# Kernel tuning notes

Measured on AMD Instinct MI355X. Metric: run time of the kernel, lower is better.

Reference implementation:

```python
import jax, jax.numpy as jnp
import numpy as np

B, T, D, H, F = 2, 128, 256, 8, 64
C = H * F          # channels = 512
TEMB = 512         # time_embed_dim


def setup_inputs() -> dict:
    key = jax.random.key(0)
    ks = jax.random.split(key, 9)
    qk = jax.random.normal(ks[0], (B, D, H, T, F), jnp.float32)
    # integer-valued relative distances in [-(T-1), T-1], stored as float
    pairwise_distances = jax.random.randint(ks[1], (B, T, T), -(T - 1), T).astype(jnp.float32)
    temb = jax.random.normal(ks[2], (B, T, TEMB), jnp.float32)
    # linear layer params (note: original zero-inits w_out/b_out; we use random
    # values so the kernel correctness test is non-trivial)
    w_dist = jax.random.normal(ks[3], (C, 3), jnp.float32) / np.sqrt(3.0)
    b_dist = jax.random.normal(ks[4], (C,), jnp.float32) * 0.02
    w_time = jax.random.normal(ks[5], (C, TEMB), jnp.float32) / np.sqrt(TEMB)
    b_time = jax.random.normal(ks[6], (C,), jnp.float32) * 0.02
    w_out = jax.random.normal(ks[7], (C, C), jnp.float32) / np.sqrt(C)
    b_out = jax.random.normal(ks[8], (C,), jnp.float32) * 0.02
    return {"qk": qk, "pairwise_distances": pairwise_distances, "temb": temb,
            "w_dist": w_dist, "b_dist": b_dist, "w_time": w_time, "b_time": b_time,
            "w_out": w_out, "b_out": b_out}


def _rpe_net(pd, temb, w_dist, b_dist, w_time, b_time, w_out, b_out):
    # distance features: [B,T,T,3]
    dist_embs = jnp.stack([
        jnp.log1p(jnp.maximum(pd, 0.0)),
        jnp.log1p(jnp.maximum(-pd, 0.0)),
        (pd == 0).astype(pd.dtype),
    ], axis=-1)
    # [B,T,1,C] + [B,T,T,C]
    temb_emb = jnp.einsum('btk,ck->btc', temb, w_time) + b_time
    emb = temb_emb[:, :, None, :] + jnp.einsum('btsk,ck->btsc', dist_embs, w_dist) + b_dist
    r = jnp.einsum('btsc,oc->btso', jax.nn.silu(emb), w_out) + b_out
    return r.reshape(B, T, T, H, F)  # [B,T,S,H,F]


def reference(qk, pairwise_distances, temb, w_dist, b_dist, w_time, b_time, w_out, b_out):
    R = _rpe_net(pairwise_distances, temb, w_dist, b_dist, w_time, b_time, w_out, b_out)
    # mode == 'qk'
    return jnp.einsum('bdhtf,btshf->bdhts', qk, R)
```

## Files before the change

### kernel.cpp

```cpp
#include <hip/hip_runtime.h>
#include <hip/hip_bf16.h>
#include <math.h>

typedef __attribute__((ext_vector_type(8))) short short8;
typedef __attribute__((ext_vector_type(4))) float f32x4;

#define B_    2
#define T_    128
#define D_    256
#define H_    8
#define F_    64
#define C_    512
#define TEMB_ 512

static __device__ __forceinline__ unsigned short f2bf(float f) {
  __hip_bfloat16 h = __float2bfloat16(f);
  return reinterpret_cast<unsigned short&>(h);
}
static __device__ __forceinline__ unsigned int pk2(float a, float b) {
  return (unsigned int)f2bf(a) | ((unsigned int)f2bf(b) << 16);
}

__global__ __launch_bounds__(256) void k_prep(
    const float* __restrict__ w_out, const float* __restrict__ w_dist,
    short* __restrict__ wsw, float* __restrict__ wd4)
{
  int gid = blockIdx.x * 256 + threadIdx.x;
  for (int s = gid; s < 32768; s += 16384) {
    int oi = s >> 10, rem = s & 1023, kjg = rem >> 6, l = rem & 63;
    int o = oi * 16 + (l & 15), c = kjg * 32 + (l >> 4) * 8;
    const float* src = w_out + (size_t)o * C_ + c;
    float4 a = *reinterpret_cast<const float4*>(src);
    float4 b = *reinterpret_cast<const float4*>(src + 4);
    uint4 v; v.x = pk2(a.x, a.y); v.y = pk2(a.z, a.w);
    v.z = pk2(b.x, b.y); v.w = pk2(b.z, b.w);
    *reinterpret_cast<uint4*>(wsw + (size_t)s * 8) = v;
  }
  if (gid < C_) {
    wd4[gid * 4 + 0] = w_dist[gid * 3 + 0];
    wd4[gid * 4 + 1] = w_dist[gid * 3 + 1];
    wd4[gid * 4 + 2] = w_dist[gid * 3 + 2];
    wd4[gid * 4 + 3] = 0.f;
  }
}

__global__ __launch_bounds__(256) void k_base(
    const float* __restrict__ temb, const float* __restrict__ w_time,
    const float* __restrict__ b_time, const float* __restrict__ b_dist,
    float* __restrict__ base)
{
  __shared__ float tt[32][64];
  __shared__ float wt[64][65];
  const int bt0 = blockIdx.x * 32;
  const int c0  = blockIdx.y * 64;
  const int tid = threadIdx.x;
  const int cl  = tid & 63;
  const int g   = tid >> 6;
  float acc[8] = {0.f,0.f,0.f,0.f,0.f,0.f,0.f,0.f};

  for (int k0 = 0; k0 < TEMB_; k0 += 64) {
#pragma unroll
    for (int i = 0; i < 8; ++i) {
      int idx = tid + i * 256; int r = idx >> 6, k = idx & 63;
      tt[r][k] = temb[(size_t)(bt0 + r) * TEMB_ + k0 + k];
    }
#pragma unroll
    for (int i = 0; i < 16; ++i) {
      int idx = tid + i * 256; int r = idx >> 6, k = idx & 63;
      wt[r][k] = w_time[(size_t)(c0 + r) * TEMB_ + k0 + k];
    }
    __syncthreads();
#pragma unroll
    for (int k = 0; k < 64; ++k) {
      float w = wt[cl][k];
#pragma unroll
      for (int j = 0; j < 8; ++j) acc[j] += tt[g + 4 * j][k] * w;
    }
    __syncthreads();
  }
  float bb = b_time[c0 + cl] + b_dist[c0 + cl];
#pragma unroll
  for (int j = 0; j < 8; ++j)
    base[(size_t)(bt0 + g + 4 * j) * C_ + c0 + cl] = acc[j] + bb;
}

__global__ __launch_bounds__(512, 2) void k_fused(
    const float* __restrict__ qk, const float* __restrict__ pd,
    const float* __restrict__ base, const float* __restrict__ wd4,
    const short* __restrict__ wsw, const float* __restrict__ b_out,
    float* __restrict__ out)
{
  __shared__ __align__(16) unsigned short Rlds[T_ * C_];
  __shared__ __align__(16) short At[8192];
  __shared__ float df[3][T_];

  const int bt = blockIdx.x;
  const int b  = bt >> 7;
  const int t  = bt & 127;
  const int tid  = threadIdx.x;
  const int lane = tid & 63;
  const int wave = tid >> 6;
  const int lanem = lane & 15;
  const int laneg = lane >> 4;

  if (tid < T_) {
    float p = pd[((size_t)b * T_ + t) * T_ + tid];
    df[0][tid] = log1pf(fmaxf(p, 0.f));
    df[1][tid] = log1pf(fmaxf(-p, 0.f));
    df[2][tid] = (p == 0.f) ? 1.f : 0.f;
  }

  const int wm = wave >> 2;
  const int wn = wave & 3;

  const int s_low = tid & 15;
  const int cg    = (tid >> 4) & 7;
  const int si_b  = (tid >> 7) * 2;
  const int kjA   = cg >> 2;
  const int cgl   = cg & 3;
  const int laneslotA = s_low + 16 * cgl;
  const float* baserow = base + (size_t)bt * C_;

  f32x4 acc[4][8];
#pragma unroll
  for (int mi = 0; mi < 4; ++mi)
#pragma unroll
    for (int ni = 0; ni < 8; ++ni) acc[mi][ni] = (f32x4){0.f, 0.f, 0.f, 0.f};

  for (int kt = 0; kt < 8; ++kt) {
    __syncthreads();
    short8 b0[8], b1[8];
    const int kjg0 = kt * 2, kjg1 = kt * 2 + 1;
#pragma unroll
    for (int ni = 0; ni < 8; ++ni)
      b0[ni] = *reinterpret_cast<const short8*>(
          wsw + ((size_t)((wn * 8 + ni) * 16 + kjg0) * 64 + lane) * 8);
    {
      const int cglob = kt * 64 + cg * 8;
      float4 bv0 = *reinterpret_cast<const float4*>(baserow + cglob);
      float4 bv1 = *reinterpret_cast<const float4*>(baserow + cglob + 4);
      float bs[8] = {bv0.x, bv0.y, bv0.z, bv0.w, bv1.x, bv1.y, bv1.z, bv1.w};
      float4 w[8];
#pragma unroll
      for (int j = 0; j < 8; ++j)
        w[j] = *reinterpret_cast<const float4*>(wd4 + (size_t)(cglob + j) * 4);
#pragma unroll
      for (int q = 0; q < 2; ++q) {
        int si = si_b + q;
        int s  = si * 16 + s_low;
        float d0 = df[0][s], d1 = df[1][s], d2 = df[2][s];
        float sl[8];
#pragma unroll
        for (int j = 0; j < 8; ++j) {
          float x = bs[j] + d0 * w[j].x + d1 * w[j].y + d2 * w[j].z;
          sl[j] = x / (1.f + __expf(-x));
        }
        uint4 v; v.x = pk2(sl[0], sl[1]); v.y = pk2(sl[2], sl[3]);
        v.z = pk2(sl[4], sl[5]); v.w = pk2(sl[6], sl[7]);
        *reinterpret_cast<uint4*>(&At[((si * 2 + kjA) * 64 + laneslotA) * 8]) = v;
      }
    }
#pragma unroll
    for (int ni = 0; ni < 8; ++ni)
      b1[ni] = *reinterpret_cast<const short8*>(
          wsw + ((size_t)((wn * 8 + ni) * 16 + kjg1) * 64 + lane) * 8);
    __syncthreads();
    short8 a0[4], a1[4];
#pragma unroll
    for (int mi = 0; mi < 4; ++mi)
      a0[mi] = *reinterpret_cast<const short8*>(
          &At[(((wm * 4 + mi) * 2 + 0) * 64 + lane) * 8]);
#pragma unroll
    for (int ni = 0; ni < 8; ++ni)
#pragma unroll
      for (int mi = 0; mi < 4; ++mi)
        acc[mi][ni] = __builtin_amdgcn_mfma_f32_16x16x32_bf16(
            a0[mi], b0[ni], acc[mi][ni], 0, 0, 0);
#pragma unroll
    for (int mi = 0; mi < 4; ++mi)
      a1[mi] = *reinterpret_cast<const short8*>(
          &At[(((wm * 4 + mi) * 2 + 1) * 64 + lane) * 8]);
#pragma unroll
    for (int ni = 0; ni < 8; ++ni)
#pragma unroll
      for (int mi = 0; mi < 4; ++mi)
        acc[mi][ni] = __builtin_amdgcn_mfma_f32_16x16x32_bf16(
            a1[mi], b1[ni], acc[mi][ni], 0, 0, 0);
  }

#pragma unroll
  for (int ni = 0; ni < 8; ++ni) {
    const int o  = wn * 128 + ni * 16 + lanem;
    const float bo = b_out[o];
    const int g  = o >> 3;
#pragma unroll
    for (int mi = 0; mi < 4; ++mi) {
#pragma unroll
      for (int reg = 0; reg < 4; ++reg) {
        int s  = wm * 64 + mi * 16 + laneg * 4 + reg;
        int gp = (g & ~7) | ((g ^ s) & 7);
        Rlds[s * 512 + gp * 8 + (o & 7)] = f2bf(acc[mi][ni][reg] + bo);
      }
    }
  }
  __syncthreads();

  const int h = wave;
  short8 brf[2][8];
#pragma unroll
  for (int kj = 0; kj < 2; ++kj)
#pragma unroll
    for (int ni = 0; ni < 8; ++ni) {
      int s  = ni * 16 + lanem;
      int g  = h * 8 + kj * 4 + laneg;
      int gp = (g & ~7) | ((g ^ s) & 7);
      brf[kj][ni] = *reinterpret_cast<const short8*>(&Rlds[s * 512 + gp * 8]);
    }

  const int HTF = H_ * T_ * F_;
  const int HTT = H_ * T_ * T_;
  const float* qkb = qk + (size_t)b * D_ * HTF + (size_t)h * T_ * F_ + (size_t)t * F_;
  float* outb = out + (size_t)b * D_ * HTT + (size_t)h * T_ * T_ + (size_t)t * T_;

  auto LOADC = [&](int d0, float4* buf) {
#pragma unroll
    for (int mi = 0; mi < 2; ++mi) {
      const float* src = qkb + (size_t)(d0 + mi * 16 + lanem) * HTF + laneg * 8;
      buf[mi * 4 + 0] = *reinterpret_cast<const float4*>(src);
      buf[mi * 4 + 1] = *reinterpret_cast<const float4*>(src + 4);
      buf[mi * 4 + 2] = *reinterpret_cast<const float4*>(src + 32);
      buf[mi * 4 + 3] = *reinterpret_cast<const float4*>(src + 36);
    }
  };
  auto COMP = [&](int d0, const float4* buf) {
    f32x4 ac[2][8];
#pragma unroll
    for (int mi = 0; mi < 2; ++mi)
#pragma unroll
      for (int ni = 0; ni < 8; ++ni) ac[mi][ni] = (f32x4){0.f, 0.f, 0.f, 0.f};
#pragma unroll
    for (int kj = 0; kj < 2; ++kj) {
      short8 av[2];
#pragma unroll
      for (int mi = 0; mi < 2; ++mi) {
        float4 p0 = buf[mi * 4 + kj * 2], p1 = buf[mi * 4 + kj * 2 + 1];
        union { uint4 u; short8 s; } cv;
        cv.u.x = pk2(p0.x, p0.y); cv.u.y = pk2(p0.z, p0.w);
        cv.u.z = pk2(p1.x, p1.y); cv.u.w = pk2(p1.z, p1.w);
        av[mi] = cv.s;
      }
#pragma unroll
      for (int ni = 0; ni < 8; ++ni)
#pragma unroll
        for (int mi = 0; mi < 2; ++mi)
          ac[mi][ni] = __builtin_amdgcn_mfma_f32_16x16x32_bf16(
              av[mi], brf[kj][ni], ac[mi][ni], 0, 0, 0);
    }
#pragma unroll
    for (int mi = 0; mi < 2; ++mi)
#pragma unroll
      for (int reg = 0; reg < 4; ++reg) {
        float* row = outb + (size_t)(d0 + mi * 16 + laneg * 4 + reg) * HTT;
#pragma unroll
        for (int ni = 0; ni < 8; ++ni)
          row[ni * 16 + lanem] = ac[mi][ni][reg];
      }
  };

  float4 bufA[8], bufB[8];
  LOADC(0, bufA);
#pragma unroll
  for (int cc = 0; cc < 4; ++cc) {
    LOADC(cc * 64 + 32, bufB);
    COMP(cc * 64, bufA);
    if (cc < 3) LOADC(cc * 64 + 64, bufA);
    COMP(cc * 64 + 32, bufB);
  }
}

extern "C" void kernel_launch(void* const* d_in, const int* in_sizes, int n_in,
                              void* d_out, int out_size, void* d_ws, size_t ws_size,
                              hipStream_t stream) {
  const float* qk     = (const float*)d_in[0];
  const float* pd     = (const float*)d_in[1];
  const float* temb   = (const float*)d_in[2];
  const float* w_dist = (const float*)d_in[3];
  const float* b_dist = (const float*)d_in[4];
  const float* w_time = (const float*)d_in[5];
  const float* b_time = (const float*)d_in[6];
  const float* w_out  = (const float*)d_in[7];
  const float* b_out  = (const float*)d_in[8];
  float* out = (float*)d_out;

  char* ws = (char*)d_ws;
  float* base = (float*)(ws);
  float* wd4  = (float*)(ws + 524288);
  short* wsw  = (short*)(ws + 532480);

  hipLaunchKernelGGL(k_prep, dim3(64), dim3(256), 0, stream,
                     w_out, w_dist, wsw, wd4);
  hipLaunchKernelGGL(k_base, dim3(8, 8), dim3(256), 0, stream,
                     temb, w_time, b_time, b_dist, base);
  hipLaunchKernelGGL(k_fused, dim3(B_ * T_), dim3(512), 0, stream,
                     qk, pd, base, wd4, wsw, b_out, out);
}
```

Baseline: 174.7 us.

## Double fused kernel block to 1024 threads and split work across sixteen waves

The fused kernel now launches 1024 threads per block, so sixteen waves each own half the output columns in the R GEMM and half the D range per head in the final qk contraction. The distance-weight table is transposed so each thread reads it with vector loads, and every thread builds one A-tile row instead of two. The first qk tile is loaded before the barrier, and the qk loop becomes a single-buffered prefetch over 16-row chunks. More waves per block should hide latency better, but the register budget per thread is tighter under the 1024-thread launch bound, and only 256 blocks run on a chip with many CUs.

Measured after the change: 196.2 us. 1.12x slower.

```diff
diff --git a/kernel.cpp b/kernel.cpp
--- a/kernel.cpp
+++ b/kernel.cpp
@@ -23,7 +23,7 @@
 
 __global__ __launch_bounds__(256) void k_prep(
     const float* __restrict__ w_out, const float* __restrict__ w_dist,
-    short* __restrict__ wsw, float* __restrict__ wd4)
+    short* __restrict__ wsw, float* __restrict__ wdT)
 {
   int gid = blockIdx.x * 256 + threadIdx.x;
   for (int s = gid; s < 32768; s += 16384) {
@@ -37,10 +37,9 @@
     *reinterpret_cast<uint4*>(wsw + (size_t)s * 8) = v;
   }
   if (gid < C_) {
-    wd4[gid * 4 + 0] = w_dist[gid * 3 + 0];
-    wd4[gid * 4 + 1] = w_dist[gid * 3 + 1];
-    wd4[gid * 4 + 2] = w_dist[gid * 3 + 2];
-    wd4[gid * 4 + 3] = 0.f;
+    wdT[0 * C_ + gid] = w_dist[gid * 3 + 0];
+    wdT[1 * C_ + gid] = w_dist[gid * 3 + 1];
+    wdT[2 * C_ + gid] = w_dist[gid * 3 + 2];
   }
 }
 
@@ -84,9 +83,9 @@
     base[(size_t)(bt0 + g + 4 * j) * C_ + c0 + cl] = acc[j] + bb;
 }
 
-__global__ __launch_bounds__(512, 2) void k_fused(
+__global__ __launch_bounds__(1024, 4) void k_fused(
     const float* __restrict__ qk, const float* __restrict__ pd,
-    const float* __restrict__ base, const float* __restrict__ wd4,
+    const float* __restrict__ base, const float* __restrict__ wdT,
     const short* __restrict__ wsw, const float* __restrict__ b_out,
     float* __restrict__ out)
 {
@@ -110,87 +109,96 @@
     df[2][tid] = (p == 0.f) ? 1.f : 0.f;
   }
 
-  const int wm = wave >> 2;
-  const int wn = wave & 3;
+  const int wm = wave >> 3;
+  const int wn = wave & 7;
 
   const int s_low = tid & 15;
   const int cg    = (tid >> 4) & 7;
-  const int si_b  = (tid >> 7) * 2;
+  const int si    = tid >> 7;
   const int kjA   = cg >> 2;
   const int cgl   = cg & 3;
   const int laneslotA = s_low + 16 * cgl;
+  const int sA    = si * 16 + s_low;
   const float* baserow = base + (size_t)bt * C_;
 
-  f32x4 acc[4][8];
+  f32x4 acc[4][4];
 #pragma unroll
   for (int mi = 0; mi < 4; ++mi)
 #pragma unroll
-    for (int ni = 0; ni < 8; ++ni) acc[mi][ni] = (f32x4){0.f, 0.f, 0.f, 0.f};
+    for (int ni = 0; ni < 4; ++ni) acc[mi][ni] = (f32x4){0.f, 0.f, 0.f, 0.f};
 
   for (int kt = 0; kt < 8; ++kt) {
     __syncthreads();
-    short8 b0[8], b1[8];
-    const int kjg0 = kt * 2, kjg1 = kt * 2 + 1;
-#pragma unroll
-    for (int ni = 0; ni < 8; ++ni)
+    short8 b0[4], b1[4];
+#pragma unroll
+    for (int ni = 0; ni < 4; ++ni)
       b0[ni] = *reinterpret_cast<const short8*>(
-          wsw + ((size_t)((wn * 8 + ni) * 16 + kjg0) * 64 + lane) * 8);
+          wsw + ((size_t)((wn * 4 + ni) * 16 + kt * 2 + 0) * 64 + lane) * 8);
     {
       const int cglob = kt * 64 + cg * 8;
-      float4 bv0 = *reinterpret_cast<const float4*>(baserow + cglob);
-      float4 bv1 = *reinterpret_cast<const float4*>(baserow + cglob + 4);
-      float bs[8] = {bv0.x, bv0.y, bv0.z, bv0.w, bv1.x, bv1.y, bv1.z, bv1.w};
-      float4 w[8];
-#pragma unroll
-      for (int j = 0; j < 8; ++j)
-        w[j] = *reinterpret_cast<const float4*>(wd4 + (size_t)(cglob + j) * 4);
-#pragma unroll
-      for (int q = 0; q < 2; ++q) {
-        int si = si_b + q;
-        int s  = si * 16 + s_low;
-        float d0 = df[0][s], d1 = df[1][s], d2 = df[2][s];
-        float sl[8];
-#pragma unroll
-        for (int j = 0; j < 8; ++j) {
-          float x = bs[j] + d0 * w[j].x + d1 * w[j].y + d2 * w[j].z;
-          sl[j] = x / (1.f + __expf(-x));
-        }
-        uint4 v; v.x = pk2(sl[0], sl[1]); v.y = pk2(sl[2], sl[3]);
-        v.z = pk2(sl[4], sl[5]); v.w = pk2(sl[6], sl[7]);
-        *reinterpret_cast<uint4*>(&At[((si * 2 + kjA) * 64 + laneslotA) * 8]) = v;
+      const float d0 = df[0][sA], d1 = df[1][sA], d2 = df[2][sA];
+      uint4 v;
+      {
+        float4 bs = *reinterpret_cast<const float4*>(baserow + cglob);
+        float4 wa = *reinterpret_cast<const float4*>(wdT + cglob);
+        float4 wb = *reinterpret_cast<const float4*>(wdT + C_ + cglob);
+        float4 wc = *reinterpret_cast<const float4*>(wdT + 2 * C_ + cglob);
+        float x0 = bs.x + d0 * wa.x + d1 * wb.x + d2 * wc.x;
+        float x1 = bs.y + d0 * wa.y + d1 * wb.y + d2 * wc.y;
+        float x2 = bs.z + d0 * wa.z + d1 * wb.z + d2 * wc.z;
+        float x3 = bs.w + d0 * wa.w + d1 * wb.w + d2 * wc.w;
+        x0 = x0 / (1.f + __expf(-x0)); x1 = x1 / (1.f + __expf(-x1));
+        x2 = x2 / (1.f + __expf(-x2)); x3 = x3 / (1.f + __expf(-x3));
+        v.x = pk2(x0, x1); v.y = pk2(x2, x3);
       }
-    }
-#pragma unroll
-    for (int ni = 0; ni < 8; ++ni)
+      {
+        float4 bs = *reinterpret_cast<const float4*>(baserow + cglob + 4);
+        float4 wa = *reinterpret_cast<const float4*>(wdT + cglob + 4);
+        float4 wb = *reinterpret_cast<const float4*>(wdT + C_ + cglob + 4);
+        float4 wc = *reinterpret_cast<const float4*>(wdT + 2 * C_ + cglob + 4);
+        float x0 = bs.x + d0 * wa.x + d1 * wb.x + d2 * wc.x;
+        float x1 = bs.y + d0 * wa.y + d1 * wb.y + d2 * wc.y;
+        float x2 = bs.z + d0 * wa.z + d1 * wb.z + d2 * wc.z;
+        float x3 = bs.w + d0 * wa.w + d1 * wb.w + d2 * wc.w;
+        x0 = x0 / (1.f + __expf(-x0)); x1 = x1 / (1.f + __expf(-x1));
+        x2 = x2 / (1.f + __expf(-x2)); x3 = x3 / (1.f + __expf(-x3));
+        v.z = pk2(x0, x1); v.w = pk2(x2, x3);
+      }
+      *reinterpret_cast<uint4*>(&At[((si * 2 + kjA) * 64 + laneslotA) * 8]) = v;
+    }
+#pragma unroll
+    for (int ni = 0; ni < 4; ++ni)
       b1[ni] = *reinterpret_cast<const short8*>(
-          wsw + ((size_t)((wn * 8 + ni) * 16 + kjg1) * 64 + lane) * 8);
+          wsw + ((size_t)((wn * 4 + ni) * 16 + kt * 2 + 1) * 64 + lane) * 8);
     __syncthreads();
-    short8 a0[4], a1[4];
-#pragma unroll
-    for (int mi = 0; mi < 4; ++mi)
-      a0[mi] = *reinterpret_cast<const short8*>(
-          &At[(((wm * 4 + mi) * 2 + 0) * 64 + lane) * 8]);
-#pragma unroll
-    for (int ni = 0; ni < 8; ++ni)
+    {
+      short8 a[4];
 #pragma unroll
       for (int mi = 0; mi < 4; ++mi)
-        acc[mi][ni] = __builtin_amdgcn_mfma_f32_16x16x32_bf16(
-            a0[mi], b0[ni], acc[mi][ni], 0, 0, 0);
-#pragma unroll
-    for (int mi = 0; mi < 4; ++mi)
-      a1[mi] = *reinterpret_cast<const short8*>(
-          &At[(((wm * 4 + mi) * 2 + 1) * 64 + lane) * 8]);
-#pragma unroll
-    for (int ni = 0; ni < 8; ++ni)
+        a[mi] = *reinterpret_cast<const short8*>(
+            &At[(((wm * 4 + mi) * 2 + 0) * 64 + lane) * 8]);
+#pragma unroll
+      for (int ni = 0; ni < 4; ++ni)
+#pragma unroll
+        for (int mi = 0; mi < 4; ++mi)
+          acc[mi][ni] = __builtin_amdgcn_mfma_f32_16x16x32_bf16(
+              a[mi], b0[ni], acc[mi][ni], 0, 0, 0);
 #pragma unroll
       for (int mi = 0; mi < 4; ++mi)
-        acc[mi][ni] = __builtin_amdgcn_mfma_f32_16x16x32_bf16(
-            a1[mi], b1[ni], acc[mi][ni], 0, 0, 0);
-  }
-
-#pragma unroll
-  for (int ni = 0; ni < 8; ++ni) {
-    const int o  = wn * 128 + ni * 16 + lanem;
+        a[mi] = *reinterpret_cast<const short8*>(
+            &At[(((wm * 4 + mi) * 2 + 1) * 64 + lane) * 8]);
+#pragma unroll
+      for (int ni = 0; ni < 4; ++ni)
+#pragma unroll
+        for (int mi = 0; mi < 4; ++mi)
+          acc[mi][ni] = __builtin_amdgcn_mfma_f32_16x16x32_bf16(
+              a[mi], b1[ni], acc[mi][ni], 0, 0, 0);
+    }
+  }
+
+#pragma unroll
+  for (int ni = 0; ni < 4; ++ni) {
+    const int o  = wn * 64 + ni * 16 + lanem;
     const float bo = b_out[o];
     const int g  = o >> 3;
 #pragma unroll
@@ -203,9 +211,24 @@
       }
     }
   }
+
+  const int h  = wave >> 1;
+  const int dh = wave & 1;
+  const size_t HTF = (size_t)H_ * T_ * F_;
+  const size_t HTT = (size_t)H_ * T_ * T_;
+  const float* qkb = qk + (size_t)b * D_ * HTF + (size_t)h * T_ * F_ + (size_t)t * F_;
+  float* outb = out + (size_t)b * D_ * HTT + (size_t)h * T_ * T_ + (size_t)t * T_;
+
+  float4 buf[4];
+  {
+    const float* src = qkb + (size_t)(dh * 128 + lanem) * HTF + laneg * 8;
+    buf[0] = *reinterpret_cast<const float4*>(src);
+    buf[1] = *reinterpret_cast<const float4*>(src + 4);
+    buf[2] = *reinterpret_cast<const float4*>(src + 32);
+    buf[3] = *reinterpret_cast<const float4*>(src + 36);
+  }
   __syncthreads();
 
-  const int h = wave;
   short8 brf[2][8];
 #pragma unroll
   for (int kj = 0; kj < 2; ++kj)
@@ -217,64 +240,41 @@
       brf[kj][ni] = *reinterpret_cast<const short8*>(&Rlds[s * 512 + gp * 8]);
     }
 
-  const int HTF = H_ * T_ * F_;
-  const int HTT = H_ * T_ * T_;
-  const float* qkb = qk + (size_t)b * D_ * HTF + (size_t)h * T_ * F_ + (size_t)t * F_;
-  float* outb = out + (size_t)b * D_ * HTT + (size_t)h * T_ * T_ + (size_t)t * T_;
-
-  auto LOADC = [&](int d0, float4* buf) {
-#pragma unroll
-    for (int mi = 0; mi < 2; ++mi) {
-      const float* src = qkb + (size_t)(d0 + mi * 16 + lanem) * HTF + laneg * 8;
-      buf[mi * 4 + 0] = *reinterpret_cast<const float4*>(src);
-      buf[mi * 4 + 1] = *reinterpret_cast<const float4*>(src + 4);
-      buf[mi * 4 + 2] = *reinterpret_cast<const float4*>(src + 32);
-      buf[mi * 4 + 3] = *reinterpret_cast<const float4*>(src + 36);
-    }
-  };
-  auto COMP = [&](int d0, const float4* buf) {
-    f32x4 ac[2][8];
-#pragma unroll
-    for (int mi = 0; mi < 2; ++mi)
-#pragma unroll
-      for (int ni = 0; ni < 8; ++ni) ac[mi][ni] = (f32x4){0.f, 0.f, 0.f, 0.f};
-#pragma unroll
-    for (int kj = 0; kj < 2; ++kj) {
-      short8 av[2];
-#pragma unroll
-      for (int mi = 0; mi < 2; ++mi) {
-        float4 p0 = buf[mi * 4 + kj * 2], p1 = buf[mi * 4 + kj * 2 + 1];
-        union { uint4 u; short8 s; } cv;
-        cv.u.x = pk2(p0.x, p0.y); cv.u.y = pk2(p0.z, p0.w);
-        cv.u.z = pk2(p1.x, p1.y); cv.u.w = pk2(p1.z, p1.w);
-        av[mi] = cv.s;
-      }
+  for (int cc = 0; cc < 8; ++cc) {
+    const int dbase = dh * 128 + cc * 16;
+    short8 av0, av1;
+    {
+      union { uint4 u; short8 s; } cv;
+      cv.u.x = pk2(buf[0].x, buf[0].y); cv.u.y = pk2(buf[0].z, buf[0].w);
+      cv.u.z = pk2(buf[1].x, buf[1].y); cv.u.w = pk2(buf[1].z, buf[1].w);
+      av0 = cv.s;
+      cv.u.x = pk2(buf[2].x, buf[2].y); cv.u.y = pk2(buf[2].z, buf[2].w);
+      cv.u.z = pk2(buf[3].x, buf[3].y); cv.u.w = pk2(buf[3].z, buf[3].w);
+      av1 = cv.s;
+    }
+    if (cc < 7) {
+      const float* src = qkb + (size_t)(dbase + 16 + lanem) * HTF + laneg * 8;
+      buf[0] = *reinterpret_cast<const float4*>(src);
+      buf[1] = *reinterpret_cast<const float4*>(src + 4);
+      buf[2] = *reinterpret_cast<const float4*>(src + 32);
+      buf[3] = *reinterpret_cast<const float4*>(src + 36);
+    }
+    f32x4 ac[8];
+#pragma unroll
+    for (int ni = 0; ni < 8; ++ni) ac[ni] = (f32x4){0.f, 0.f, 0.f, 0.f};
+#pragma unroll
+    for (int ni = 0; ni < 8; ++ni)
+      ac[ni] = __builtin_amdgcn_mfma_f32_16x16x32_bf16(av0, brf[0][ni], ac[ni], 0, 0, 0);
+#pragma unroll
+    for (int ni = 0; ni < 8; ++ni)
+      ac[ni] = __builtin_amdgcn_mfma_f32_16x16x32_bf16(av1, brf[1][ni], ac[ni], 0, 0, 0);
+#pragma unroll
+    for (int reg = 0; reg < 4; ++reg) {
+      float* row = outb + (size_t)(dbase + laneg * 4 + reg) * HTT;
 #pragma unroll
       for (int ni = 0; ni < 8; ++ni)
-#pragma unroll
-        for (int mi = 0; mi < 2; ++mi)
-          ac[mi][ni] = __builtin_amdgcn_mfma_f32_16x16x32_bf16(
-              av[mi], brf[kj][ni], ac[mi][ni], 0, 0, 0);
-    }
-#pragma unroll
-    for (int mi = 0; mi < 2; ++mi)
-#pragma unroll
-      for (int reg = 0; reg < 4; ++reg) {
-        float* row = outb + (size_t)(d0 + mi * 16 + laneg * 4 + reg) * HTT;
-#pragma unroll
-        for (int ni = 0; ni < 8; ++ni)
-          row[ni * 16 + lanem] = ac[mi][ni][reg];
-      }
-  };
-
-  float4 bufA[8], bufB[8];
-  LOADC(0, bufA);
-#pragma unroll
-  for (int cc = 0; cc < 4; ++cc) {
-    LOADC(cc * 64 + 32, bufB);
-    COMP(cc * 64, bufA);
-    if (cc < 3) LOADC(cc * 64 + 64, bufA);
-    COMP(cc * 64 + 32, bufB);
+        row[ni * 16 + lanem] = ac[ni][reg];
+    }
   }
 }
 
@@ -294,13 +294,13 @@
 
   char* ws = (char*)d_ws;
   float* base = (float*)(ws);
-  float* wd4  = (float*)(ws + 524288);
+  float* wdT  = (float*)(ws + 524288);
   short* wsw  = (short*)(ws + 532480);
 
   hipLaunchKernelGGL(k_prep, dim3(64), dim3(256), 0, stream,
-                     w_out, w_dist, wsw, wd4);
+                     w_out, w_dist, wsw, wdT);
   hipLaunchKernelGGL(k_base, dim3(8, 8), dim3(256), 0, stream,
                      temb, w_time, b_time, b_dist, base);
-  hipLaunchKernelGGL(k_fused, dim3(B_ * T_), dim3(512), 0, stream,
-                     qk, pd, base, wd4, wsw, b_out, out);
-}
+  hipLaunchKernelGGL(k_fused, dim3(B_ * T_), dim3(1024), 0, stream,
+                     qk, pd, base, wdT, wsw, b_out, out);
+}
```
